# Kernel optimization log

Hardware: AMD Instinct MI355X
Metric: run time of the kernel (lower is better)

The kernel has to match this reference:

```python
import jax, jax.numpy as jnp
import numpy as np

B, T = 32, 128
NQ, NC, DK, DA = 1000, 64, 128, 128


def _xavier(k, shape):
    bound = float(np.sqrt(6.0 / (shape[0] + shape[1])))
    return jax.random.uniform(k, shape, jnp.float32, -bound, bound)


def setup_inputs() -> dict:
    key = jax.random.key(0)
    ks = jax.random.split(key, 12)
    q_data = jax.random.randint(ks[0], (B, T), 0, NQ)
    a_data = (jax.random.uniform(ks[1], (B, T)) < 0.5).astype(jnp.float32)
    q_matrix = (jax.random.uniform(ks[2], (NQ + 10, NC)) < 0.1).astype(jnp.float32)
    q_embed_w = _xavier(ks[3], (NQ + 10, DK))
    W1 = _xavier(ks[4], (DK, DA + DK)); b1 = jnp.zeros((DK,), jnp.float32)
    W2 = _xavier(ks[5], (DK, 3 * DK)); b2 = jnp.zeros((DK,), jnp.float32)
    W3 = _xavier(ks[6], (DK, 3 * DK)); b3 = jnp.zeros((DK,), jnp.float32)
    W4 = _xavier(ks[7], (DK, 2 * DK)); b4 = jnp.zeros((DK,), jnp.float32)
    W5 = _xavier(ks[8], (DK, 2 * DK)); b5 = jnp.zeros((DK,), jnp.float32)
    h0 = _xavier(ks[9], (NC, DK))  # xavier init of the per-concept memory, shared across batch
    return dict(q_data=q_data, a_data=a_data, q_matrix=q_matrix, q_embed_w=q_embed_w,
                W1=W1, b1=b1, W2=W2, b2=b2, W3=W3, b3=b3, W4=W4, b4=b4, W5=W5, b5=b5, h0=h0)


def reference(q_data, a_data, q_matrix, q_embed_w, W1, b1, W2, b2, W3, b3, W4, b4, W5, b5, h0):
    Bn, Tn = q_data.shape
    dk = W1.shape[0]
    q_emb = q_embed_w[q_data]                                    # [B,T,dk]
    a_rep = jnp.broadcast_to(a_data[:, :, None], (Bn, Tn, DA))   # a repeated along d_a
    qa = jnp.concatenate([q_emb, a_rep], -1) @ W1.T + b1         # [B,T,dk]
    qm = q_matrix[q_data]                                        # [B,T,n_c]
    h_pre0 = jnp.broadcast_to(h0, (Bn,) + h0.shape)              # [B,n_c,dk]
    h_tilde0 = jnp.einsum('bn,bnd->bd', qm[:, 0], h_pre0)        # t=0 lazy init of h_tilde_pre
    learning0 = jnp.zeros((Bn, dk), q_emb.dtype)

    def step(carry, xs):
        learning_pre, h_pre, h_tilde_pre = carry
        q_e, q_e_next, learning, qemb_next = xs
        cat3 = jnp.concatenate([learning_pre, learning, h_tilde_pre], -1)  # [B,3dk]
        KP = jnp.tanh(cat3 @ W2.T + b2)
        R = jax.nn.sigmoid(cat3 @ W3.T + b3)
        KC = R * (KP + 1.0) * 0.5                                # [B,dk]
        KC_tilde = q_e[:, :, None] * KC[:, None, :]              # outer-product memory write [B,n_c,dk]
        KC_b = jnp.broadcast_to(KC[:, None, :], h_pre.shape)
        KR = jax.nn.sigmoid(jnp.concatenate([h_pre, KC_b], -1) @ W4.T + b4) * h_pre
        h = KC_tilde + KR                                        # [B,n_c,dk]
        h_tilde = jnp.einsum('bn,bnd->bd', q_e_next, h)          # memory read for next item
        y = jax.nn.sigmoid(jnp.concatenate([qemb_next, h_tilde], -1) @ W5.T + b5).sum(-1) / dk
        return (learning, h, h_tilde), (h_pre, y)

    xs = (jnp.swapaxes(qm[:, :-1], 0, 1),    # q_e for t=0..T-2
          jnp.swapaxes(qm[:, 1:], 0, 1),     # q_e at t+1
          jnp.swapaxes(qa[:, :-1], 0, 1),    # learning_t
          jnp.swapaxes(q_emb[:, 1:], 0, 1))  # q_embed at t+1
    _, (H, ys) = jax.lax.scan(step, (learning0, h_pre0, h_tilde0), xs)
    H = jax.nn.sigmoid(H)                                        # [T-1,B,n_c,dk], matches torch stacking
    pred = jnp.concatenate([jnp.zeros((Bn, 1), ys.dtype), ys.T], axis=1)  # pred[:,0]=0
    return (H, pred, q_emb, qa)
```

## Files before the change

### kernel.cpp

```cpp
#include <hip/hip_runtime.h>

#define B_  32
#define T_  128
#define HBS 136

typedef __attribute__((ext_vector_type(8))) short bf16x8;
typedef __attribute__((ext_vector_type(4))) float f32x4;
typedef __attribute__((ext_vector_type(8))) unsigned short u16x8;

__device__ __forceinline__ float sigf(float x){ return __builtin_amdgcn_rcpf(1.f + __expf(-x)); }
__device__ __forceinline__ float tanh_f(float x){ return 2.f*__builtin_amdgcn_rcpf(1.f + __expf(-2.f*x)) - 1.f; }
__device__ __forceinline__ unsigned short f2b(float x){
  union { float f; unsigned int u; } v; v.f = x;
  return (unsigned short)((v.u + 0x7FFFu + ((v.u >> 16) & 1u)) >> 16);
}
__device__ __forceinline__ float b2f(unsigned short u){
  union { unsigned int x; float f; } v; v.x = ((unsigned int)u) << 16; return v.f;
}
__device__ __forceinline__ void bar_lds(){
  __builtin_amdgcn_sched_barrier(0);
  asm volatile("s_waitcnt lgkmcnt(0)" ::: "memory");
  __builtin_amdgcn_s_barrier();
  __builtin_amdgcn_sched_barrier(0);
}

__global__ __launch_bounds__(256) void stage_k(
    const float* __restrict__ W2, const float* __restrict__ W3,
    const float* __restrict__ W4, const float* __restrict__ W1,
    unsigned short* __restrict__ W2b, unsigned short* __restrict__ W3b,
    unsigned short* __restrict__ W4b, float* __restrict__ S)
{
  int i = blockIdx.x*256 + threadIdx.x;
  if (i < 128*384){ W2b[i] = f2b(W2[i]); W3b[i] = f2b(W3[i]); }
  if (i < 128*256){ W4b[i] = f2b(W4[i]); }
  if (i < 128){
    float s = 0.f;
    const float* row = W1 + (size_t)i*256 + 128;
    for (int k = 0; k < 128; ++k) s += row[k];
    S[i] = s;
  }
}

__global__ __launch_bounds__(256) void prep_k(
    const int* __restrict__ qd, const float* __restrict__ ad,
    const float* __restrict__ qew, const float* __restrict__ W1,
    const float* __restrict__ b1, const float* __restrict__ S,
    float* __restrict__ oqe, float* __restrict__ oqa, float* __restrict__ pred)
{
  __shared__ float qe[16][128];
  __shared__ float w1c[128][65];
  const int tid = threadIdx.x;
  const int bt0 = blockIdx.x * 16;

  for (int i = tid; i < 16*128; i += 256){
    int r = i >> 7, d = i & 127;
    float v = qew[(size_t)qd[bt0 + r]*128 + d];
    qe[r][d] = v;
    oqe[(size_t)(bt0 + r)*128 + d] = v;
  }
  const int j = tid & 127, rh = tid >> 7;
  float accv[8];
  {
    float base = b1[j], Sj = S[j];
#pragma unroll
    for (int r = 0; r < 8; ++r) accv[r] = fmaf(ad[bt0 + rh*8 + r], Sj, base);
  }
  for (int c = 0; c < 2; ++c){
    __syncthreads();
    for (int i = tid; i < 128*64; i += 256){
      int jj = i >> 6, kk = i & 63;
      w1c[jj][kk] = W1[(size_t)jj*256 + c*64 + kk];
    }
    __syncthreads();
#pragma unroll 4
    for (int k = 0; k < 64; ++k){
      float wv = w1c[j][k];
#pragma unroll
      for (int r = 0; r < 8; ++r) accv[r] = fmaf(qe[rh*8 + r][c*64 + k], wv, accv[r]);
    }
  }
#pragma unroll
  for (int r = 0; r < 8; ++r) oqa[(size_t)(bt0 + rh*8 + r)*128 + j] = accv[r];
  if (blockIdx.x == 0 && tid < 32) pred[tid * T_] = 0.f;
}

__global__ __launch_bounds__(512) void l23_k(
    const float* __restrict__ oqa,
    const unsigned short* __restrict__ W2b, const unsigned short* __restrict__ W3b,
    const float* __restrict__ b2, const float* __restrict__ b3,
    unsigned short* __restrict__ L2b, unsigned short* __restrict__ L3b)
{
  __shared__ unsigned short qab[129*136];
  const int b = blockIdx.x, tid = threadIdx.x;
  const int w = tid >> 6, lane = tid & 63, g = lane >> 4, li = lane & 15;
  const int mw = w & 3, nw = w >> 2;

  for (int i = tid; i < 129*128; i += 512){
    int row = i >> 7, k = i & 127;
    qab[row*136 + k] = row ? f2b(oqa[((size_t)b*T_ + row-1)*128 + k]) : (unsigned short)0;
  }
  __syncthreads();

  const unsigned short* Wp[2] = {W2b, W3b};
  const float*          bp[2] = {b2, b3};
  unsigned short*       Lp[2] = {L2b, L3b};
#pragma unroll
  for (int m_ = 0; m_ < 2; ++m_){
    bf16x8 bfr[4][8];
#pragma unroll
    for (int nt4 = 0; nt4 < 4; ++nt4){
      int j = (nw*4 + nt4)*16 + li;
#pragma unroll
      for (int ks = 0; ks < 8; ++ks)
        bfr[nt4][ks] = *(const bf16x8*)(Wp[m_] + (size_t)j*384 + ks*32 + 8*g);
    }
    f32x4 acc[2][4] = {{{0,0,0,0},{0,0,0,0},{0,0,0,0},{0,0,0,0}},
                       {{0,0,0,0},{0,0,0,0},{0,0,0,0},{0,0,0,0}}};
#pragma unroll
    for (int mt2 = 0; mt2 < 2; ++mt2){
      int row = (mw*2 + mt2)*16 + li;
      bf16x8 afr[8];
#pragma unroll
      for (int ks = 0; ks < 4; ++ks){
        afr[ks]   = *(const bf16x8*)&qab[ row   *136 + ks*32 + 8*g];
        afr[ks+4] = *(const bf16x8*)&qab[(row+1)*136 + ks*32 + 8*g];
      }
#pragma unroll
      for (int ks = 0; ks < 8; ++ks)
#pragma unroll
        for (int nt4 = 0; nt4 < 4; ++nt4)
          acc[mt2][nt4] = __builtin_amdgcn_mfma_f32_16x16x32_bf16(afr[ks], bfr[nt4][ks], acc[mt2][nt4], 0,0,0);
    }
    float bias[4];
#pragma unroll
    for (int nt4 = 0; nt4 < 4; ++nt4) bias[nt4] = bp[m_][(nw*4 + nt4)*16 + li];
#pragma unroll
    for (int mt2 = 0; mt2 < 2; ++mt2)
#pragma unroll
      for (int nt4 = 0; nt4 < 4; ++nt4)
#pragma unroll
        for (int r = 0; r < 4; ++r){
          int t = (mw*2 + mt2)*16 + g*4 + r;
          int j = (nw*4 + nt4)*16 + li;
          if (t < 127) Lp[m_][((size_t)b*127 + t)*128 + j] = f2b(acc[mt2][nt4][r] + bias[nt4]);
        }
  }
}

struct __align__(16) SmR {
  unsigned short hb[2][64*HBS];
  float qe[3][64];
  unsigned short htb[128];
  unsigned short kcb[128];
  int qdl[T_];
};

__global__ __launch_bounds__(512) void recur_k(
    const int* __restrict__ qd, const float* __restrict__ qmx,
    const float* __restrict__ h0, const float* __restrict__ b4,
    const unsigned short* __restrict__ W2b, const unsigned short* __restrict__ W3b,
    const unsigned short* __restrict__ W4b,
    const unsigned short* __restrict__ L2b, const unsigned short* __restrict__ L3b,
    float* __restrict__ H, unsigned short* __restrict__ HTg)
{
  __shared__ SmR s;
  const int b   = blockIdx.x;
  const int tid = threadIdx.x;
  const int w = tid >> 6, lane = tid & 63, g = lane >> 4, li = lane & 15;
  const int j = w*16 + li;

  bf16x8 w2cf[4], w3cf[4];
#pragma unroll
  for (int ks = 0; ks < 4; ++ks){
    w2cf[ks] = *(const bf16x8*)(W2b + (size_t)j*384 + 256 + ks*32 + 8*g);
    w3cf[ks] = *(const bf16x8*)(W3b + (size_t)j*384 + 256 + ks*32 + 8*g);
  }
  bf16x8 w4f[8];
#pragma unroll
  for (int ks = 0; ks < 8; ++ks)
    w4f[ks] = *(const bf16x8*)(W4b + (size_t)j*256 + ks*32 + 8*g);
  const float b4v = b4[j];

  float hreg[4][4];
#pragma unroll
  for (int mt = 0; mt < 4; ++mt)
#pragma unroll
    for (int r = 0; r < 4; ++r)
      hreg[mt][r] = h0[(mt*16 + g*4 + r)*128 + j];

  for (int i = tid; i < 64*128; i += 512){
    int n = i >> 7, d = i & 127;
    float v = h0[i];
    s.hb[0][n*HBS + d] = f2b(v);
    H[(size_t)b*8192 + i] = sigf(v);
  }
  if (tid < T_) s.qdl[tid] = qd[b*T_ + tid];
  __syncthreads();
  if (tid < 64){
    s.qe[0][tid] = qmx[(size_t)s.qdl[0]*64 + tid];
    s.qe[1][tid] = qmx[(size_t)s.qdl[1]*64 + tid];
  }
  __syncthreads();
  if (tid < 128){
    float acc = 0.f;
    for (int n = 0; n < 64; ++n) acc = fmaf(s.qe[0][n], h0[n*128 + tid], acc);
    s.htb[tid] = f2b(acc);
  }
  __syncthreads();

  float l2v = b2f(L2b[((size_t)b*127)*128 + j]);
  float l3v = b2f(L3b[((size_t)b*127)*128 + j]);
  f32x4 qc4[4];
#pragma unroll
  for (int mt = 0; mt < 4; ++mt) qc4[mt] = *(const f32x4*)&s.qe[0][mt*16 + g*4];

#pragma unroll 1
  for (int t = 0; t < T_-1; ++t){
    const int cur = t & 1, nxt = cur ^ 1;

    int tp1 = (t+1 < 127) ? t+1 : 126;
    unsigned short l2n = L2b[((size_t)b*127 + tp1)*128 + j];
    unsigned short l3n = L3b[((size_t)b*127 + tp1)*128 + j];
    float qmxv = 0.f;
    if (tid < 64 && t+2 < T_) qmxv = qmx[(size_t)s.qdl[t+2]*64 + tid];

    bf16x8 av[4];
#pragma unroll
    for (int ks = 0; ks < 4; ++ks) av[ks] = *(const bf16x8*)&s.htb[ks*32 + 8*g];
    f32x4 q2[4], q3[4];
#pragma unroll
    for (int ks = 0; ks < 4; ++ks){
      f32x4 z = {0,0,0,0};
      q2[ks] = __builtin_amdgcn_mfma_f32_16x16x32_bf16(av[ks], w2cf[ks], z, 0,0,0);
      q3[ks] = __builtin_amdgcn_mfma_f32_16x16x32_bf16(av[ks], w3cf[ks], z, 0,0,0);
    }
    float kp = tanh_f((q2[0][0]+q2[1][0]) + (q2[2][0]+q2[3][0]) + l2v);
    float rr = sigf ((q3[0][0]+q3[1][0]) + (q3[2][0]+q3[3][0]) + l3v);
    float kc = rr*(kp + 1.f)*0.5f;
    if (g == 0) s.kcb[j] = f2b(kc);

    bf16x8 af[4][4];
#pragma unroll
    for (int mt = 0; mt < 4; ++mt)
#pragma unroll
      for (int ks = 0; ks < 4; ++ks)
        af[mt][ks] = *(const bf16x8*)&s.hb[cur][(mt*16 + li)*HBS + ks*32 + 8*g];
    f32x4 acc[4] = {{0,0,0,0},{0,0,0,0},{0,0,0,0},{0,0,0,0}};
#pragma unroll
    for (int ks = 0; ks < 4; ++ks)
#pragma unroll
      for (int mt = 0; mt < 4; ++mt)
        acc[mt] = __builtin_amdgcn_mfma_f32_16x16x32_bf16(af[mt][ks], w4f[ks], acc[mt], 0,0,0);

    if (t >= 1){
      unsigned short* Hu = (unsigned short*)(H + ((size_t)t*B_ + b)*8192);
#pragma unroll
      for (int k = 0; k < 2; ++k){
        int c = tid + k*512;
        int n = c >> 4, o = (c & 15)*8;
        u16x8 hv = *(const u16x8*)&s.hb[cur][n*HBS + o];
        *(u16x8*)&Hu[c*8] = hv;
      }
    }
    f32x4 qn4[4];
#pragma unroll
    for (int mt = 0; mt < 4; ++mt)
      qn4[mt] = *(const f32x4*)&s.qe[(t+1)%3][mt*16 + g*4];
    bar_lds();

    bf16x8 kf[4];
#pragma unroll
    for (int ks = 0; ks < 4; ++ks) kf[ks] = *(const bf16x8*)&s.kcb[ks*32 + 8*g];
    f32x4 zk[4];
#pragma unroll
    for (int ks = 0; ks < 4; ++ks){
      f32x4 z = {0,0,0,0};
      zk[ks] = __builtin_amdgcn_mfma_f32_16x16x32_bf16(kf[ks], w4f[ks+4], z, 0,0,0);
    }
    float ack = (zk[0][0]+zk[1][0]) + (zk[2][0]+zk[3][0]);

    float part = 0.f;
#pragma unroll
    for (int mt = 0; mt < 4; ++mt){
#pragma unroll
      for (int r = 0; r < 4; ++r){
        int n = mt*16 + g*4 + r;
        float sg = sigf(acc[mt][r] + ack + b4v);
        float hn = fmaf(qc4[mt][r], kc, sg*hreg[mt][r]);
        hreg[mt][r] = hn;
        s.hb[nxt][n*HBS + j] = f2b(hn);
        part = fmaf(qn4[mt][r], hn, part);
      }
    }
    part += __shfl_xor(part, 16);
    part += __shfl_xor(part, 32);
    if (g == 0){
      unsigned short hb16 = f2b(part);
      s.htb[j] = hb16;
      HTg[((size_t)b*T_ + t + 1)*128 + j] = hb16;
    }
    if (tid < 64 && t+2 < T_) s.qe[(t+2)%3][tid] = qmxv;
    l2v = b2f(l2n); l3v = b2f(l3n);
#pragma unroll
    for (int mt = 0; mt < 4; ++mt) qc4[mt] = qn4[mt];
    bar_lds();
  }
}

__global__ __launch_bounds__(256) void hexp_k(float* __restrict__ H)
{
  const int tb = blockIdx.x;
  const int t  = (tb >> 5) + 1, b = tb & 31;
  float* Hs = H + ((size_t)t*B_ + b)*8192;
  const unsigned short* Hu = (const unsigned short*)Hs;
  const int tid = threadIdx.x;

  u16x8 v[4];
#pragma unroll
  for (int k = 0; k < 4; ++k){
    int c = k*256 + tid;
    v[k] = *(const u16x8*)&Hu[c*8];
  }
  __syncthreads();
#pragma unroll
  for (int k = 0; k < 4; ++k){
    int c = k*256 + tid;
    f32x4 lo, hi;
    lo[0]=sigf(b2f(v[k][0])); lo[1]=sigf(b2f(v[k][1]));
    lo[2]=sigf(b2f(v[k][2])); lo[3]=sigf(b2f(v[k][3]));
    hi[0]=sigf(b2f(v[k][4])); hi[1]=sigf(b2f(v[k][5]));
    hi[2]=sigf(b2f(v[k][6])); hi[3]=sigf(b2f(v[k][7]));
    *(f32x4*)&Hs[c*8]     = lo;
    *(f32x4*)&Hs[c*8 + 4] = hi;
  }
}

__global__ __launch_bounds__(256) void ypost_k(
    const float* __restrict__ oqe, const unsigned short* __restrict__ HT,
    const float* __restrict__ W5, const float* __restrict__ b5,
    float* __restrict__ pred)
{
  __shared__ float X[32][256];
  __shared__ float w5c[128][33];
  const int tau = blockIdx.x + 1;
  const int tid = threadIdx.x;

  for (int i = tid; i < 32*128; i += 256){
    int bb = i >> 7, k = i & 127;
    X[bb][k] = oqe[((size_t)bb*T_ + tau)*128 + k];
    X[bb][128 + k] = b2f(HT[((size_t)bb*T_ + tau)*128 + k]);
  }
  const int j = tid & 127, rh = tid >> 7;
  float acc[16];
  float base = b5[j];
#pragma unroll
  for (int r = 0; r < 16; ++r) acc[r] = base;
  for (int c = 0; c < 8; ++c){
    __syncthreads();
    for (int i = tid; i < 128*32; i += 256){
      int jj = i >> 5, kk = i & 31;
      w5c[jj][kk] = W5[(size_t)jj*256 + c*32 + kk];
    }
    __syncthreads();
#pragma unroll 8
    for (int k = 0; k < 32; ++k){
      float wv = w5c[j][k];
#pragma unroll
      for (int r = 0; r < 16; ++r) acc[r] = fmaf(X[rh*16 + r][c*32 + k], wv, acc[r]);
    }
  }
  __syncthreads();
#pragma unroll
  for (int r = 0; r < 16; ++r) X[rh*16 + r][j] = sigf(acc[r]);
  __syncthreads();
  if (tid < 32){
    float ssum = 0.f;
    for (int k = 0; k < 128; ++k) ssum += X[tid][k];
    pred[tid*T_ + tau] = ssum * (1.f/128.f);
  }
}

extern "C" void kernel_launch(void* const* d_in, const int* in_sizes, int n_in,
                              void* d_out, int out_size, void* d_ws, size_t ws_size,
                              hipStream_t stream)
{
  const int*   qd  = (const int*)  d_in[0];
  const float* ad  = (const float*)d_in[1];
  const float* qmx = (const float*)d_in[2];
  const float* qew = (const float*)d_in[3];
  const float* W1  = (const float*)d_in[4];
  const float* b1  = (const float*)d_in[5];
  const float* W2  = (const float*)d_in[6];
  const float* b2  = (const float*)d_in[7];
  const float* W3  = (const float*)d_in[8];
  const float* b3  = (const float*)d_in[9];
  const float* W4  = (const float*)d_in[10];
  const float* b4  = (const float*)d_in[11];
  const float* W5  = (const float*)d_in[12];
  const float* b5  = (const float*)d_in[13];
  const float* h0  = (const float*)d_in[14];

  float* H    = (float*)d_out;
  float* pred = H    + (size_t)127*32*64*128;
  float* oqe  = pred + (size_t)32*128;
  float* oqa  = oqe  + (size_t)32*128*128;

  unsigned short* W2b = (unsigned short*)d_ws;
  unsigned short* W3b = W2b + 128*384;
  unsigned short* W4b = W3b + 128*384;
  unsigned short* HTg = W4b + 128*256;
  unsigned short* L2b = HTg + (size_t)32*128*128;
  unsigned short* L3b = L2b + (size_t)32*127*128;
  float*          S   = (float*)(L3b + (size_t)32*127*128);

  stage_k<<<192, 256, 0, stream>>>(W2, W3, W4, W1, W2b, W3b, W4b, S);
  prep_k <<<256, 256, 0, stream>>>(qd, ad, qew, W1, b1, S, oqe, oqa, pred);
  l23_k  <<<32,  512, 0, stream>>>(oqa, W2b, W3b, b2, b3, L2b, L3b);
  recur_k<<<32,  512, 0, stream>>>(qd, qmx, h0, b4, W2b, W3b, W4b,
                                   L2b, L3b, H, HTg);
  hexp_k <<<126*32, 256, 0, stream>>>(H);
  ypost_k<<<127, 256, 0, stream>>>(oqe, HTg, W5, b5, pred);
}
```

Measured before the change: 371.1 us.

## Split l23 across time, interleave L2/L3, fuse post kernels, tighten recurrence step

The l23 precompute now runs on 128 blocks (4 time chunks per batch) instead of 32, and it writes the W2 and W3 input projections interleaved as packed bf16 pairs, so each recurrence step needs one 32-bit load. Inside the recurrent loop, tanh and sigmoid are combined into a single reciprocal of a product of exponentials. The KC/W4 partial matvec is moved ahead of the H stores, and new hidden values are packed with v_cvt_pk_bf16_f32. The sigmoid-expansion and prediction kernels are merged into one launch to save a launch and let the two kinds of work overlap. The serial recurrence kernel remains the dominant cost, and the fused KC formula may overflow or lose accuracy for extreme inputs.

```diff
diff --git a/kernel.cpp b/kernel.cpp
--- a/kernel.cpp
+++ b/kernel.cpp
@@ -9,7 +9,6 @@
 typedef __attribute__((ext_vector_type(8))) unsigned short u16x8;
 
 __device__ __forceinline__ float sigf(float x){ return __builtin_amdgcn_rcpf(1.f + __expf(-x)); }
-__device__ __forceinline__ float tanh_f(float x){ return 2.f*__builtin_amdgcn_rcpf(1.f + __expf(-2.f*x)) - 1.f; }
 __device__ __forceinline__ unsigned short f2b(float x){
   union { float f; unsigned int u; } v; v.f = x;
   return (unsigned short)((v.u + 0x7FFFu + ((v.u >> 16) & 1u)) >> 16);
@@ -88,62 +87,68 @@
     const float* __restrict__ oqa,
     const unsigned short* __restrict__ W2b, const unsigned short* __restrict__ W3b,
     const float* __restrict__ b2, const float* __restrict__ b3,
-    unsigned short* __restrict__ L2b, unsigned short* __restrict__ L3b)
-{
-  __shared__ unsigned short qab[129*136];
-  const int b = blockIdx.x, tid = threadIdx.x;
+    unsigned short* __restrict__ LIb)
+{
+  __shared__ unsigned short qab[33*136];
+  const int blk = blockIdx.x;
+  const int b = blk >> 2, t0 = (blk & 3) * 32;
+  const int tid = threadIdx.x;
   const int w = tid >> 6, lane = tid & 63, g = lane >> 4, li = lane & 15;
-  const int mw = w & 3, nw = w >> 2;
-
-  for (int i = tid; i < 129*128; i += 512){
+  const int mt = w & 1, ng = w >> 1;
+
+  for (int i = tid; i < 33*128; i += 512){
     int row = i >> 7, k = i & 127;
-    qab[row*136 + k] = row ? f2b(oqa[((size_t)b*T_ + row-1)*128 + k]) : (unsigned short)0;
-  }
-  __syncthreads();
-
-  const unsigned short* Wp[2] = {W2b, W3b};
-  const float*          bp[2] = {b2, b3};
-  unsigned short*       Lp[2] = {L2b, L3b};
+    int tt = t0 - 1 + row;
+    qab[row*136 + k] = (tt >= 0) ? f2b(oqa[((size_t)b*T_ + tt)*128 + k]) : (unsigned short)0;
+  }
+  __syncthreads();
+
+  bf16x8 afr[8];
+  {
+    int row = mt*16 + li;
+#pragma unroll
+    for (int ks = 0; ks < 4; ++ks){
+      afr[ks]   = *(const bf16x8*)&qab[ row   *136 + ks*32 + 8*g];
+      afr[ks+4] = *(const bf16x8*)&qab[(row+1)*136 + ks*32 + 8*g];
+    }
+  }
+  const int nt[2] = { ng, ng + 4 };
+  float o2r[2][4];
 #pragma unroll
   for (int m_ = 0; m_ < 2; ++m_){
-    bf16x8 bfr[4][8];
-#pragma unroll
-    for (int nt4 = 0; nt4 < 4; ++nt4){
-      int j = (nw*4 + nt4)*16 + li;
-#pragma unroll
-      for (int ks = 0; ks < 8; ++ks)
-        bfr[nt4][ks] = *(const bf16x8*)(Wp[m_] + (size_t)j*384 + ks*32 + 8*g);
-    }
-    f32x4 acc[2][4] = {{{0,0,0,0},{0,0,0,0},{0,0,0,0},{0,0,0,0}},
-                       {{0,0,0,0},{0,0,0,0},{0,0,0,0},{0,0,0,0}}};
-#pragma unroll
-    for (int mt2 = 0; mt2 < 2; ++mt2){
-      int row = (mw*2 + mt2)*16 + li;
-      bf16x8 afr[8];
-#pragma unroll
-      for (int ks = 0; ks < 4; ++ks){
-        afr[ks]   = *(const bf16x8*)&qab[ row   *136 + ks*32 + 8*g];
-        afr[ks+4] = *(const bf16x8*)&qab[(row+1)*136 + ks*32 + 8*g];
+    const unsigned short* Wp = m_ ? W3b : W2b;
+    const float*          bp = m_ ? b3  : b2;
+    f32x4 acc[2] = {{0,0,0,0},{0,0,0,0}};
+#pragma unroll
+    for (int u = 0; u < 2; ++u){
+      int j = nt[u]*16 + li;
+      const unsigned short* wr = Wp + (size_t)j*384;
+#pragma unroll
+      for (int ks = 0; ks < 8; ++ks){
+        bf16x8 bb = *(const bf16x8*)(wr + ks*32 + 8*g);
+        acc[u] = __builtin_amdgcn_mfma_f32_16x16x32_bf16(afr[ks], bb, acc[u], 0,0,0);
       }
-#pragma unroll
-      for (int ks = 0; ks < 8; ++ks)
-#pragma unroll
-        for (int nt4 = 0; nt4 < 4; ++nt4)
-          acc[mt2][nt4] = __builtin_amdgcn_mfma_f32_16x16x32_bf16(afr[ks], bfr[nt4][ks], acc[mt2][nt4], 0,0,0);
-    }
-    float bias[4];
-#pragma unroll
-    for (int nt4 = 0; nt4 < 4; ++nt4) bias[nt4] = bp[m_][(nw*4 + nt4)*16 + li];
-#pragma unroll
-    for (int mt2 = 0; mt2 < 2; ++mt2)
-#pragma unroll
-      for (int nt4 = 0; nt4 < 4; ++nt4)
+    }
+#pragma unroll
+    for (int u = 0; u < 2; ++u){
+      float bias = bp[nt[u]*16 + li];
+      if (m_ == 0){
+#pragma unroll
+        for (int r = 0; r < 4; ++r) o2r[u][r] = acc[u][r] + bias;
+      } else {
 #pragma unroll
         for (int r = 0; r < 4; ++r){
-          int t = (mw*2 + mt2)*16 + g*4 + r;
-          int j = (nw*4 + nt4)*16 + li;
-          if (t < 127) Lp[m_][((size_t)b*127 + t)*128 + j] = f2b(acc[mt2][nt4][r] + bias[nt4]);
+          int t = t0 + mt*16 + g*4 + r;
+          int j = nt[u]*16 + li;
+          if (t < 127){
+            unsigned int p;
+            float l3f = acc[u][r] + bias;
+            asm("v_cvt_pk_bf16_f32 %0, %1, %2" : "=v"(p) : "v"(o2r[u][r]), "v"(l3f));
+            *(unsigned int*)&LIb[(((size_t)b*127 + t)*128 + j)*2] = p;
+          }
         }
+      }
+    }
   }
 }
 
@@ -160,7 +165,7 @@
     const float* __restrict__ h0, const float* __restrict__ b4,
     const unsigned short* __restrict__ W2b, const unsigned short* __restrict__ W3b,
     const unsigned short* __restrict__ W4b,
-    const unsigned short* __restrict__ L2b, const unsigned short* __restrict__ L3b,
+    const unsigned short* __restrict__ LIb,
     float* __restrict__ H, unsigned short* __restrict__ HTg)
 {
   __shared__ SmR s;
@@ -208,8 +213,8 @@
   }
   __syncthreads();
 
-  float l2v = b2f(L2b[((size_t)b*127)*128 + j]);
-  float l3v = b2f(L3b[((size_t)b*127)*128 + j]);
+  unsigned int lv = *(const unsigned int*)&LIb[(((size_t)b*127)*128 + j)*2];
+  float l2v = b2f((unsigned short)lv), l3v = b2f((unsigned short)(lv >> 16));
   f32x4 qc4[4];
 #pragma unroll
   for (int mt = 0; mt < 4; ++mt) qc4[mt] = *(const f32x4*)&s.qe[0][mt*16 + g*4];
@@ -219,8 +224,7 @@
     const int cur = t & 1, nxt = cur ^ 1;
 
     int tp1 = (t+1 < 127) ? t+1 : 126;
-    unsigned short l2n = L2b[((size_t)b*127 + tp1)*128 + j];
-    unsigned short l3n = L3b[((size_t)b*127 + tp1)*128 + j];
+    unsigned int ln = *(const unsigned int*)&LIb[(((size_t)b*127 + tp1)*128 + j)*2];
     float qmxv = 0.f;
     if (tid < 64 && t+2 < T_) qmxv = qmx[(size_t)s.qdl[t+2]*64 + tid];
 
@@ -234,9 +238,9 @@
       q2[ks] = __builtin_amdgcn_mfma_f32_16x16x32_bf16(av[ks], w2cf[ks], z, 0,0,0);
       q3[ks] = __builtin_amdgcn_mfma_f32_16x16x32_bf16(av[ks], w3cf[ks], z, 0,0,0);
     }
-    float kp = tanh_f((q2[0][0]+q2[1][0]) + (q2[2][0]+q2[3][0]) + l2v);
-    float rr = sigf ((q3[0][0]+q3[1][0]) + (q3[2][0]+q3[3][0]) + l3v);
-    float kc = rr*(kp + 1.f)*0.5f;
+    float o2 = (q2[0][0]+q2[1][0]) + (q2[2][0]+q2[3][0]) + l2v;
+    float o3 = (q3[0][0]+q3[1][0]) + (q3[2][0]+q3[3][0]) + l3v;
+    float kc = __builtin_amdgcn_rcpf((1.f + __expf(-o3)) * (1.f + __expf(-2.f*o2)));
     if (g == 0) s.kcb[j] = f2b(kc);
 
     bf16x8 af[4][4];
@@ -251,6 +255,23 @@
 #pragma unroll
       for (int mt = 0; mt < 4; ++mt)
         acc[mt] = __builtin_amdgcn_mfma_f32_16x16x32_bf16(af[mt][ks], w4f[ks], acc[mt], 0,0,0);
+
+    f32x4 qn4[4];
+#pragma unroll
+    for (int mt = 0; mt < 4; ++mt)
+      qn4[mt] = *(const f32x4*)&s.qe[(t+1)%3][mt*16 + g*4];
+    bar_lds();
+
+    bf16x8 kf[4];
+#pragma unroll
+    for (int ks = 0; ks < 4; ++ks) kf[ks] = *(const bf16x8*)&s.kcb[ks*32 + 8*g];
+    f32x4 zk[4];
+#pragma unroll
+    for (int ks = 0; ks < 4; ++ks){
+      f32x4 z = {0,0,0,0};
+      zk[ks] = __builtin_amdgcn_mfma_f32_16x16x32_bf16(kf[ks], w4f[ks+4], z, 0,0,0);
+    }
+    float ack = (zk[0][0]+zk[1][0]) + (zk[2][0]+zk[3][0]);
 
     if (t >= 1){
       unsigned short* Hu = (unsigned short*)(H + ((size_t)t*B_ + b)*8192);
@@ -262,89 +283,79 @@
         *(u16x8*)&Hu[c*8] = hv;
       }
     }
-    f32x4 qn4[4];
-#pragma unroll
-    for (int mt = 0; mt < 4; ++mt)
-      qn4[mt] = *(const f32x4*)&s.qe[(t+1)%3][mt*16 + g*4];
-    bar_lds();
-
-    bf16x8 kf[4];
-#pragma unroll
-    for (int ks = 0; ks < 4; ++ks) kf[ks] = *(const bf16x8*)&s.kcb[ks*32 + 8*g];
-    f32x4 zk[4];
-#pragma unroll
-    for (int ks = 0; ks < 4; ++ks){
-      f32x4 z = {0,0,0,0};
-      zk[ks] = __builtin_amdgcn_mfma_f32_16x16x32_bf16(kf[ks], w4f[ks+4], z, 0,0,0);
-    }
-    float ack = (zk[0][0]+zk[1][0]) + (zk[2][0]+zk[3][0]);
-
-    float part = 0.f;
+
+    float part[4];
 #pragma unroll
     for (int mt = 0; mt < 4; ++mt){
+      float hn[4], pp = 0.f;
 #pragma unroll
       for (int r = 0; r < 4; ++r){
-        int n = mt*16 + g*4 + r;
         float sg = sigf(acc[mt][r] + ack + b4v);
-        float hn = fmaf(qc4[mt][r], kc, sg*hreg[mt][r]);
-        hreg[mt][r] = hn;
-        s.hb[nxt][n*HBS + j] = f2b(hn);
-        part = fmaf(qn4[mt][r], hn, part);
+        float v = fmaf(qc4[mt][r], kc, sg*hreg[mt][r]);
+        hreg[mt][r] = v; hn[r] = v;
+        pp = fmaf(qn4[mt][r], v, pp);
       }
-    }
-    part += __shfl_xor(part, 16);
-    part += __shfl_xor(part, 32);
+      part[mt] = pp;
+      unsigned int p01, p23;
+      asm("v_cvt_pk_bf16_f32 %0, %1, %2" : "=v"(p01) : "v"(hn[0]), "v"(hn[1]));
+      asm("v_cvt_pk_bf16_f32 %0, %1, %2" : "=v"(p23) : "v"(hn[2]), "v"(hn[3]));
+      int n0 = mt*16 + g*4;
+      unsigned short* bp_ = &s.hb[nxt][n0*HBS + j];
+      bp_[0]       = (unsigned short)p01;
+      bp_[HBS]     = (unsigned short)(p01 >> 16);
+      bp_[2*HBS]   = (unsigned short)p23;
+      bp_[3*HBS]   = (unsigned short)(p23 >> 16);
+    }
+    float prt = (part[0]+part[1]) + (part[2]+part[3]);
+    prt += __shfl_xor(prt, 16);
+    prt += __shfl_xor(prt, 32);
     if (g == 0){
-      unsigned short hb16 = f2b(part);
+      unsigned short hb16 = f2b(prt);
       s.htb[j] = hb16;
       HTg[((size_t)b*T_ + t + 1)*128 + j] = hb16;
     }
     if (tid < 64 && t+2 < T_) s.qe[(t+2)%3][tid] = qmxv;
-    l2v = b2f(l2n); l3v = b2f(l3n);
+    lv = ln;
+    l2v = b2f((unsigned short)lv); l3v = b2f((unsigned short)(lv >> 16));
 #pragma unroll
     for (int mt = 0; mt < 4; ++mt) qc4[mt] = qn4[mt];
     bar_lds();
   }
 }
 
-__global__ __launch_bounds__(256) void hexp_k(float* __restrict__ H)
-{
-  const int tb = blockIdx.x;
-  const int t  = (tb >> 5) + 1, b = tb & 31;
-  float* Hs = H + ((size_t)t*B_ + b)*8192;
-  const unsigned short* Hu = (const unsigned short*)Hs;
-  const int tid = threadIdx.x;
-
-  u16x8 v[4];
-#pragma unroll
-  for (int k = 0; k < 4; ++k){
-    int c = k*256 + tid;
-    v[k] = *(const u16x8*)&Hu[c*8];
-  }
-  __syncthreads();
-#pragma unroll
-  for (int k = 0; k < 4; ++k){
-    int c = k*256 + tid;
-    f32x4 lo, hi;
-    lo[0]=sigf(b2f(v[k][0])); lo[1]=sigf(b2f(v[k][1]));
-    lo[2]=sigf(b2f(v[k][2])); lo[3]=sigf(b2f(v[k][3]));
-    hi[0]=sigf(b2f(v[k][4])); hi[1]=sigf(b2f(v[k][5]));
-    hi[2]=sigf(b2f(v[k][6])); hi[3]=sigf(b2f(v[k][7]));
-    *(f32x4*)&Hs[c*8]     = lo;
-    *(f32x4*)&Hs[c*8 + 4] = hi;
-  }
-}
-
-__global__ __launch_bounds__(256) void ypost_k(
+__global__ __launch_bounds__(256) void post_k(
     const float* __restrict__ oqe, const unsigned short* __restrict__ HT,
     const float* __restrict__ W5, const float* __restrict__ b5,
-    float* __restrict__ pred)
+    float* __restrict__ pred, float* __restrict__ H)
 {
   __shared__ float X[32][256];
   __shared__ float w5c[128][33];
+  const int tid = threadIdx.x;
+
+  if ((int)blockIdx.x >= 127){
+    const int tb = blockIdx.x - 127;
+    const int t  = (tb >> 5) + 1, b = tb & 31;
+    float* Hs = H + ((size_t)t*B_ + b)*8192;
+    const unsigned short* Hu = (const unsigned short*)Hs;
+    u16x8 v[4];
+#pragma unroll
+    for (int k = 0; k < 4; ++k) v[k] = *(const u16x8*)&Hu[(k*256 + tid)*8];
+    __syncthreads();
+#pragma unroll
+    for (int k = 0; k < 4; ++k){
+      int c = k*256 + tid;
+      f32x4 lo, hi;
+      lo[0]=sigf(b2f(v[k][0])); lo[1]=sigf(b2f(v[k][1]));
+      lo[2]=sigf(b2f(v[k][2])); lo[3]=sigf(b2f(v[k][3]));
+      hi[0]=sigf(b2f(v[k][4])); hi[1]=sigf(b2f(v[k][5]));
+      hi[2]=sigf(b2f(v[k][6])); hi[3]=sigf(b2f(v[k][7]));
+      *(f32x4*)&Hs[c*8]     = lo;
+      *(f32x4*)&Hs[c*8 + 4] = hi;
+    }
+    return;
+  }
+
   const int tau = blockIdx.x + 1;
-  const int tid = threadIdx.x;
-
   for (int i = tid; i < 32*128; i += 256){
     int bb = i >> 7, k = i & 127;
     X[bb][k] = oqe[((size_t)bb*T_ + tau)*128 + k];
@@ -409,15 +420,13 @@
   unsigned short* W3b = W2b + 128*384;
   unsigned short* W4b = W3b + 128*384;
   unsigned short* HTg = W4b + 128*256;
-  unsigned short* L2b = HTg + (size_t)32*128*128;
-  unsigned short* L3b = L2b + (size_t)32*127*128;
-  float*          S   = (float*)(L3b + (size_t)32*127*128);
+  unsigned short* LIb = HTg + (size_t)32*128*128;
+  float*          S   = (float*)(LIb + (size_t)32*127*128*2);
 
   stage_k<<<192, 256, 0, stream>>>(W2, W3, W4, W1, W2b, W3b, W4b, S);
   prep_k <<<256, 256, 0, stream>>>(qd, ad, qew, W1, b1, S, oqe, oqa, pred);
-  l23_k  <<<32,  512, 0, stream>>>(oqa, W2b, W3b, b2, b3, L2b, L3b);
+  l23_k  <<<128, 512, 0, stream>>>(oqa, W2b, W3b, b2, b3, LIb);
   recur_k<<<32,  512, 0, stream>>>(qd, qmx, h0, b4, W2b, W3b, W4b,
-                                   L2b, L3b, H, HTg);
-  hexp_k <<<126*32, 256, 0, stream>>>(H);
-  ypost_k<<<127, 256, 0, stream>>>(oqe, HTg, W5, b5, pred);
-}
+                                   LIb, H, HTg);
+  post_k <<<127 + 126*32, 256, 0, stream>>>(oqe, HTg, W5, b5, pred, H);
+}
```

New measurement: 336.7 us. -9.3%, faster.
